# Performance work log

Measured on AMD Instinct MI355X. Metric: run time of the kernel, lower is better.

## Reference

```python
import jax, jax.numpy as jnp
import numpy as np
from math import ceil

WIDTH, HEIGHT, NUM_TILE = 1920, 1080, 16
# NOTE: original code computes BOTH block dims from height (bug preserved for faithfulness)
BLOCK_W = ceil(HEIGHT / NUM_TILE)
BLOCK_H = ceil(HEIGHT / NUM_TILE)
T = NUM_TILE * NUM_TILE  # 256 tiles
N = 65536


def setup_inputs() -> dict:
    key = jax.random.key(0)
    k1, k2, k3 = jax.random.split(key, 3)
    pos2d = jax.random.uniform(k1, (N, 2), jnp.float32) * jnp.array([WIDTH, HEIGHT], jnp.float32)
    radius = jax.random.uniform(k2, (N,), jnp.float32) * 2.0  # radius in tile units, avg ~3x3 tile footprint
    depth = jax.random.uniform(k3, (N,), jnp.float32) * 10.0
    return {"pos2d": pos2d, "radius": radius, "depth": depth}


def _tile_binning(pos2d, radius, depth):
    minval, maxval = 0.0, NUM_TILE - 1e-5
    xmin = jnp.clip(pos2d[:, 0] / BLOCK_W - radius, minval, maxval).astype(jnp.int32)
    xmax = jnp.clip(pos2d[:, 0] / BLOCK_W + radius, minval, maxval).astype(jnp.int32)
    ymin = jnp.clip(pos2d[:, 1] / BLOCK_H - radius, minval, maxval).astype(jnp.int32)
    ymax = jnp.clip(pos2d[:, 1] / BLOCK_H + radius, minval, maxval).astype(jnp.int32)

    tr = jnp.arange(NUM_TILE, dtype=jnp.int32)
    in_x = (tr[None, :] >= xmin[:, None]) & (tr[None, :] <= xmax[:, None])  # [N, 16]
    in_y = (tr[None, :] >= ymin[:, None]) & (tr[None, :] <= ymax[:, None])  # [N, 16]
    # tile index t = xi + NUM_TILE * yi  -> mask[n, yi, xi]
    mask = (in_y[:, :, None] & in_x[:, None, :]).reshape(N, T)  # [N, T]

    # inclusive-cumsum bucket offsets (matches torch.cumsum(tile_count))
    tile_count = jnp.cumsum(mask.sum(axis=0).astype(jnp.int32)).astype(jnp.int32)  # [T]
    total = tile_count[-1]

    # flattened entry list, tile-major then primitive-index order (matches scatter loop order)
    maskT = mask.T.reshape(-1)                                   # [T*N]
    tile_id = jnp.repeat(jnp.arange(T, dtype=jnp.int32), N)      # [T*N]
    prim_id = jnp.tile(jnp.arange(N, dtype=jnp.int32), T)        # [T*N]
    depth_e = depth[prim_id]
    tile_eff = jnp.where(maskT, tile_id, T)  # invalid entries pushed past all real tiles

    # segmented depth sort: primary key tile, secondary depth, tertiary prim (stable tiebreak)
    order = jnp.lexsort((prim_id, depth_e, tile_eff))
    prim_sorted = prim_id[order]
    valid = jnp.arange(T * N) < total
    tile_indices = jnp.where(valid, prim_sorted, -1).astype(jnp.int32)  # [T*N], -1 padded
    return tile_count, tile_indices


def reference(pos2d, radius, depth):
    # Equivalent of Screen.create_tiles(pos2d, radius) followed by Screen.depth_sort(depth).
    # Returns (tile_count: inclusive cumsum bucket offsets [T],
    #          tile_indices: per-tile depth-sorted primitive ids, padded to T*N with -1).
    return _tile_binning(pos2d, radius, depth)
```

## Files before the change

kernel.cpp:

```cpp
#include <hip/hip_runtime.h>
#include <hip/hip_bf16.h>
#include <stdint.h>

#define NPRIM 65536
#define NT 16
#define T_TILES 256
#define NBKT 2048
#define BCAP 256
#define CTHR 512
#define CBLK 512
#define FILLB (CBLK - T_TILES)

typedef unsigned long long u64;
typedef unsigned int u32;

__device__ __forceinline__ u32 dbucket(float d) {
    u32 b = (u32)(d * 204.8f);
    return b > (NBKT - 1) ? (NBKT - 1) : b;
}

__global__ __launch_bounds__(256) void k_compute(
    const float2* __restrict__ pos2d, const float* __restrict__ radius,
    const float* __restrict__ depth, u64* __restrict__ keysRaw,
    u32* __restrict__ bounds, u32* __restrict__ counts,
    u32* __restrict__ bucket_count)
{
    __shared__ u32 hist[T_TILES];
    __shared__ u32 bhist[NBKT];
    int tid = threadIdx.x;
    hist[tid] = 0;
    for (int j = tid; j < NBKT; j += 256) bhist[j] = 0;
    __syncthreads();

    int base = blockIdx.x * 1024;
    const float mx = (float)(16.0 - 1e-5);
    #pragma unroll
    for (int q = 0; q < 4; ++q) {
        int i = base + q * 256 + tid;
        float2 p = pos2d[i];
        float r = radius[i];
        float fx = p.x / 68.0f;
        float fy = p.y / 68.0f;
        int xmin = (int)fminf(fmaxf(fx - r, 0.0f), mx);
        int xmax = (int)fminf(fmaxf(fx + r, 0.0f), mx);
        int ymin = (int)fminf(fmaxf(fy - r, 0.0f), mx);
        int ymax = (int)fminf(fmaxf(fy + r, 0.0f), mx);
        bounds[i] = (u32)(xmin | (xmax << 4) | (ymin << 8) | (ymax << 12));
        float d = depth[i];
        keysRaw[i] = ((u64)__float_as_uint(d) << 16) | (u32)i;
        atomicAdd(&bhist[dbucket(d)], 1u);
        for (int ty = ymin; ty <= ymax; ++ty)
            for (int tx = xmin; tx <= xmax; ++tx)
                atomicAdd(&hist[ty * NT + tx], 1u);
    }
    __syncthreads();
    if (hist[tid]) atomicAdd(&counts[tid], hist[tid]);
    for (int j = tid; j < NBKT; j += 256)
        if (bhist[j]) atomicAdd(&bucket_count[j], bhist[j]);
}

__global__ __launch_bounds__(256) void k_scan(
    const u32* __restrict__ counts, const u32* __restrict__ bucket_count,
    int* __restrict__ tile_count, u32* __restrict__ offsets,
    u32* __restrict__ bucket_base, u32* __restrict__ cursor)
{
    __shared__ u32 wsum[4];
    int tid = threadIdx.x, lane = tid & 63, wave = tid >> 6;

    u32 c8[8]; u32 sum8 = 0;
    #pragma unroll
    for (int j = 0; j < 8; ++j) { c8[j] = bucket_count[tid * 8 + j]; sum8 += c8[j]; }
    u32 v = sum8;
    #pragma unroll
    for (int d = 1; d < 64; d <<= 1) {
        u32 t = __shfl_up(v, d, 64);
        if (lane >= d) v += t;
    }
    if (lane == 63) wsum[wave] = v;
    __syncthreads();
    u32 add = 0;
    for (int w = 0; w < wave; ++w) add += wsum[w];
    u32 run = v + add - sum8;
    #pragma unroll
    for (int j = 0; j < 8; ++j) {
        bucket_base[tid * 8 + j] = run;
        cursor[tid * 8 + j] = run;
        run += c8[j];
    }
    __syncthreads();

    u32 c = counts[tid];
    v = c;
    #pragma unroll
    for (int d = 1; d < 64; d <<= 1) {
        u32 t = __shfl_up(v, d, 64);
        if (lane >= d) v += t;
    }
    if (lane == 63) wsum[wave] = v;
    __syncthreads();
    add = 0;
    for (int w = 0; w < wave; ++w) add += wsum[w];
    v += add;
    tile_count[tid] = (int)v;
    offsets[tid] = v - c;
}

__global__ __launch_bounds__(256) void k_scatter(
    const u64* __restrict__ keysRaw, u32* __restrict__ cursor,
    u64* __restrict__ keysBkt)
{
    int base = blockIdx.x * 1024;
    int tid = threadIdx.x;
    #pragma unroll
    for (int q = 0; q < 4; ++q) {
        u64 key = keysRaw[base + q * 256 + tid];
        u32 d = dbucket(__uint_as_float((u32)(key >> 16)));
        u32 pos = atomicAdd(&cursor[d], 1u);
        keysBkt[pos] = key;
    }
}

__global__ __launch_bounds__(256) void k_bsort(
    const u64* __restrict__ keysBkt, const u32* __restrict__ bucket_base,
    const u32* __restrict__ bucket_count, const u32* __restrict__ bounds,
    u32* __restrict__ entries)
{
    __shared__ u64 buf[4][BCAP];
    int tid = threadIdx.x, lane = tid & 63, wave = tid >> 6;
    int bucket = blockIdx.x * 4 + wave;
    u32 base = bucket_base[bucket];
    u32 n = bucket_count[bucket];
    if (n > BCAP) n = BCAP;
    #pragma unroll
    for (int t = 0; t < 4; ++t) {
        u32 i = (u32)lane + 64u * t;
        if (i < n) buf[wave][i] = keysBkt[base + i];
    }
    __syncthreads();
    #pragma unroll
    for (int t = 0; t < 4; ++t) {
        u32 i = (u32)lane + 64u * t;
        if (i < n) {
            u64 ki = buf[wave][i];
            u32 r = 0;
            for (u32 j = 0; j < n; ++j) r += (buf[wave][j] < ki);
            u32 prim = (u32)ki & 0xFFFFu;
            entries[base + r] = (bounds[prim] << 16) | prim;
        }
    }
}

__global__ __launch_bounds__(CTHR) void k_compact(
    const uint4* __restrict__ entries4, const u32* __restrict__ offsets,
    const int* __restrict__ tile_count, int* __restrict__ out_idx)
{
    int b = blockIdx.x;
    int tid = threadIdx.x;

    if (b >= T_TILES) {
        u32 total = (u32)tile_count[T_TILES - 1];
        const u32 end = (u32)T_TILES * (u32)NPRIM;
        u32 s4 = (total + 3u) & ~3u;
        if (b == T_TILES && tid < (int)(s4 - total)) out_idx[total + tid] = -1;
        u32 n4 = (end - s4) >> 2;
        int4* o4 = (int4*)(out_idx + s4);
        int4 m1 = make_int4(-1, -1, -1, -1);
        u32 gid = (u32)(b - T_TILES) * (u32)CTHR + (u32)tid;
        for (u32 i = gid; i < n4; i += (u32)FILLB * (u32)CTHR) o4[i] = m1;
        return;
    }

    int tile = b;
    int tx = tile & 15, ty = tile >> 4;
    int lane = tid & 63, wave = tid >> 6;
    __shared__ u32 wtot[8];
    u32 base = offsets[tile];
    u64 lmask = (1ull << lane) - 1;

    for (int c = 0; c < NPRIM / 2048; ++c) {
        uint4 e = entries4[c * CTHR + tid];
        u32 ev[4] = {e.x, e.y, e.z, e.w};
        bool m[4]; u64 bal[4];
        #pragma unroll
        for (int q = 0; q < 4; ++q) {
            u32 bb = ev[q] >> 16;
            int xmn = bb & 15, xmx = (bb >> 4) & 15;
            int ymn = (bb >> 8) & 15, ymx = (bb >> 12) & 15;
            m[q] = (tx >= xmn) && (tx <= xmx) && (ty >= ymn) && (ty <= ymx);
            bal[q] = __ballot(m[q]);
        }
        u32 wcnt = __popcll(bal[0]) + __popcll(bal[1]) + __popcll(bal[2]) + __popcll(bal[3]);
        if (lane == 0) wtot[wave] = wcnt;
        __syncthreads();
        u32 woff = base, tot = 0;
        #pragma unroll
        for (int w = 0; w < 8; ++w) {
            u32 t = wtot[w];
            woff += (w < wave) ? t : 0;
            tot += t;
        }
        u32 pre = __popcll(bal[0] & lmask) + __popcll(bal[1] & lmask)
                + __popcll(bal[2] & lmask) + __popcll(bal[3] & lmask);
        #pragma unroll
        for (int q = 0; q < 4; ++q) {
            if (m[q]) { out_idx[woff + pre] = (int)(ev[q] & 0xFFFFu); pre++; }
        }
        base += tot;
        __syncthreads();
    }
}

extern "C" void kernel_launch(void* const* d_in, const int* in_sizes, int n_in,
                              void* d_out, int out_size, void* d_ws, size_t ws_size,
                              hipStream_t stream)
{
    const float2* pos2d  = (const float2*)d_in[0];
    const float*  radius = (const float*)d_in[1];
    const float*  depth  = (const float*)d_in[2];

    int* out32        = (int*)d_out;
    int* tile_count   = out32;
    int* tile_indices = out32 + T_TILES;

    char* ws = (char*)d_ws;
    u64* keysRaw = (u64*)(ws);
    u64* keysBkt = (u64*)(ws + 512 * 1024);
    u32* bounds  = (u32*)(ws + 1024 * 1024);
    u32* counts       = (u32*)(ws + 1280 * 1024);
    u32* bucket_count = (u32*)(ws + 1280 * 1024 + 4096);
    u32* offsets      = (u32*)(ws + 1280 * 1024 + 16384);
    u32* bucket_base  = (u32*)(ws + 1280 * 1024 + 20480);
    u32* cursor       = (u32*)(ws + 1280 * 1024 + 32768);

    (void)hipMemsetAsync(counts, 0, 12288, stream);

    k_compute<<<64, 256, 0, stream>>>(pos2d, radius, depth, keysRaw, bounds,
                                      counts, bucket_count);
    k_scan<<<1, 256, 0, stream>>>(counts, bucket_count, tile_count, offsets,
                                  bucket_base, cursor);
    k_scatter<<<64, 256, 0, stream>>>(keysRaw, cursor, keysBkt);

    u32* entries = (u32*)keysRaw;
    k_bsort<<<NBKT / 4, 256, 0, stream>>>(keysBkt, bucket_base, bucket_count,
                                          bounds, entries);
    k_compact<<<CBLK, CTHR, 0, stream>>>((const uint4*)entries, offsets,
                                         tile_count, tile_indices);
}
```

Before: 127.0 us.

## Replace global atomics and scan kernel with per-block histograms and deterministic scatter

k_compute now writes per-block tile and depth-bucket histograms instead of global atomics, and stores each key's local rank within its bucket in the key's upper bits. That removes the memset and the separate single-block scan kernel. k_scatter recomputes bucket offsets from the per-block histograms and places keys without global atomic cursors. k_compact reduces and scans the tile counts itself, and now does a two-pass count-then-write over wave-owned chunks, so the per-chunk block-wide barriers are gone. In exchange, every block redundantly reads all per-block histograms, and the entries are read twice in compaction.

```diff
diff --git a/kernel.cpp b/kernel.cpp
--- a/kernel.cpp
+++ b/kernel.cpp
@@ -1,5 +1,4 @@
 #include <hip/hip_runtime.h>
-#include <hip/hip_bf16.h>
 #include <stdint.h>
 
 #define NPRIM 65536
@@ -7,6 +6,7 @@
 #define T_TILES 256
 #define NBKT 2048
 #define BCAP 256
+#define NBLK 64
 #define CTHR 512
 #define CBLK 512
 #define FILLB (CBLK - T_TILES)
@@ -22,8 +22,8 @@
 __global__ __launch_bounds__(256) void k_compute(
     const float2* __restrict__ pos2d, const float* __restrict__ radius,
     const float* __restrict__ depth, u64* __restrict__ keysRaw,
-    u32* __restrict__ bounds, u32* __restrict__ counts,
-    u32* __restrict__ bucket_count)
+    u32* __restrict__ bounds, u32* __restrict__ counts_blk,
+    u32* __restrict__ bh)
 {
     __shared__ u32 hist[T_TILES];
     __shared__ u32 bhist[NBKT];
@@ -47,29 +47,42 @@
         int ymax = (int)fminf(fmaxf(fy + r, 0.0f), mx);
         bounds[i] = (u32)(xmin | (xmax << 4) | (ymin << 8) | (ymax << 12));
         float d = depth[i];
-        keysRaw[i] = ((u64)__float_as_uint(d) << 16) | (u32)i;
-        atomicAdd(&bhist[dbucket(d)], 1u);
+        u32 lrank = atomicAdd(&bhist[dbucket(d)], 1u);
+        keysRaw[i] = ((u64)lrank << 48) | ((u64)__float_as_uint(d) << 16) | (u32)i;
         for (int ty = ymin; ty <= ymax; ++ty)
             for (int tx = xmin; tx <= xmax; ++tx)
                 atomicAdd(&hist[ty * NT + tx], 1u);
     }
     __syncthreads();
-    if (hist[tid]) atomicAdd(&counts[tid], hist[tid]);
-    for (int j = tid; j < NBKT; j += 256)
-        if (bhist[j]) atomicAdd(&bucket_count[j], bhist[j]);
-}
-
-__global__ __launch_bounds__(256) void k_scan(
-    const u32* __restrict__ counts, const u32* __restrict__ bucket_count,
-    int* __restrict__ tile_count, u32* __restrict__ offsets,
-    u32* __restrict__ bucket_base, u32* __restrict__ cursor)
-{
+    counts_blk[blockIdx.x * 256 + tid] = hist[tid];
+    for (int j = tid; j < NBKT; j += 256) bh[blockIdx.x * NBKT + j] = bhist[j];
+}
+
+__global__ __launch_bounds__(256) void k_scatter(
+    const u64* __restrict__ keysRaw, const u32* __restrict__ bh,
+    u64* __restrict__ keysBkt, u32* __restrict__ bucket_base,
+    u32* __restrict__ bucket_count)
+{
+    __shared__ u32 loff[NBKT];
     __shared__ u32 wsum[4];
     int tid = threadIdx.x, lane = tid & 63, wave = tid >> 6;
-
-    u32 c8[8]; u32 sum8 = 0;
-    #pragma unroll
-    for (int j = 0; j < 8; ++j) { c8[j] = bucket_count[tid * 8 + j]; sum8 += c8[j]; }
+    int blk = blockIdx.x;
+
+    u32 c8[8] = {0,0,0,0,0,0,0,0};
+    u32 p8[8] = {0,0,0,0,0,0,0,0};
+    for (int b = 0; b < NBLK; ++b) {
+        const uint4* row = (const uint4*)(bh + b * NBKT + tid * 8);
+        uint4 h0 = row[0], h1 = row[1];
+        u32 h[8] = {h0.x, h0.y, h0.z, h0.w, h1.x, h1.y, h1.z, h1.w};
+        #pragma unroll
+        for (int j = 0; j < 8; ++j) {
+            if (b < blk) p8[j] += h[j];
+            c8[j] += h[j];
+        }
+    }
+    u32 sum8 = 0;
+    #pragma unroll
+    for (int j = 0; j < 8; ++j) sum8 += c8[j];
     u32 v = sum8;
     #pragma unroll
     for (int d = 1; d < 64; d <<= 1) {
@@ -83,40 +96,22 @@
     u32 run = v + add - sum8;
     #pragma unroll
     for (int j = 0; j < 8; ++j) {
-        bucket_base[tid * 8 + j] = run;
-        cursor[tid * 8 + j] = run;
+        loff[tid * 8 + j] = run + p8[j];
+        if (blk == 0) {
+            bucket_base[tid * 8 + j] = run;
+            bucket_count[tid * 8 + j] = c8[j];
+        }
         run += c8[j];
     }
     __syncthreads();
 
-    u32 c = counts[tid];
-    v = c;
-    #pragma unroll
-    for (int d = 1; d < 64; d <<= 1) {
-        u32 t = __shfl_up(v, d, 64);
-        if (lane >= d) v += t;
-    }
-    if (lane == 63) wsum[wave] = v;
-    __syncthreads();
-    add = 0;
-    for (int w = 0; w < wave; ++w) add += wsum[w];
-    v += add;
-    tile_count[tid] = (int)v;
-    offsets[tid] = v - c;
-}
-
-__global__ __launch_bounds__(256) void k_scatter(
-    const u64* __restrict__ keysRaw, u32* __restrict__ cursor,
-    u64* __restrict__ keysBkt)
-{
-    int base = blockIdx.x * 1024;
-    int tid = threadIdx.x;
+    int base = blk * 1024;
     #pragma unroll
     for (int q = 0; q < 4; ++q) {
         u64 key = keysRaw[base + q * 256 + tid];
         u32 d = dbucket(__uint_as_float((u32)(key >> 16)));
-        u32 pos = atomicAdd(&cursor[d], 1u);
-        keysBkt[pos] = key;
+        u32 lrank = (u32)(key >> 48);
+        keysBkt[loff[d] + lrank] = key & 0x0000FFFFFFFFFFFFull;
     }
 }
 
@@ -151,14 +146,45 @@
 }
 
 __global__ __launch_bounds__(CTHR) void k_compact(
-    const uint4* __restrict__ entries4, const u32* __restrict__ offsets,
-    const int* __restrict__ tile_count, int* __restrict__ out_idx)
-{
-    int b = blockIdx.x;
-    int tid = threadIdx.x;
+    const uint4* __restrict__ entries4, const u32* __restrict__ counts_blk,
+    int* __restrict__ tile_count, int* __restrict__ out_idx)
+{
+    __shared__ u32 cnt[T_TILES];
+    __shared__ u32 excl[T_TILES];
+    __shared__ u32 wsum[4];
+    __shared__ u32 chunkcnt[64];
+    __shared__ u32 chunkoff[64];
+    int b = blockIdx.x, tid = threadIdx.x, lane = tid & 63, wave = tid >> 6;
+
+    if (tid < 256) {
+        u32 s = 0;
+        for (int bb = 0; bb < NBLK; ++bb) s += counts_blk[bb * 256 + tid];
+        cnt[tid] = s;
+    }
+    __syncthreads();
+    if (tid < 256) {
+        u32 c = cnt[tid], v = c;
+        #pragma unroll
+        for (int d = 1; d < 64; d <<= 1) {
+            u32 t = __shfl_up(v, d, 64);
+            if (lane >= d) v += t;
+        }
+        if (lane == 63) wsum[wave] = v;
+        excl[tid] = v;
+    }
+    __syncthreads();
+    if (tid < 256) {
+        u32 add = 0;
+        for (int w = 0; w < wave; ++w) add += wsum[w];
+        u32 incl = excl[tid] + add;
+        excl[tid] = incl - cnt[tid];
+        cnt[tid] = incl;
+        if (b == 0) tile_count[tid] = (int)incl;
+    }
+    __syncthreads();
+    u32 total = cnt[T_TILES - 1];
 
     if (b >= T_TILES) {
-        u32 total = (u32)tile_count[T_TILES - 1];
         const u32 end = (u32)T_TILES * (u32)NPRIM;
         u32 s4 = (total + 3u) & ~3u;
         if (b == T_TILES && tid < (int)(s4 - total)) out_idx[total + tid] = -1;
@@ -170,43 +196,63 @@
         return;
     }
 
-    int tile = b;
-    int tx = tile & 15, ty = tile >> 4;
-    int lane = tid & 63, wave = tid >> 6;
-    __shared__ u32 wtot[8];
-    u32 base = offsets[tile];
+    int tile = b, tx = tile & 15, ty = tile >> 4;
+    u32 base0 = excl[tile];
     u64 lmask = (1ull << lane) - 1;
 
-    for (int c = 0; c < NPRIM / 2048; ++c) {
-        uint4 e = entries4[c * CTHR + tid];
-        u32 ev[4] = {e.x, e.y, e.z, e.w};
-        bool m[4]; u64 bal[4];
-        #pragma unroll
-        for (int q = 0; q < 4; ++q) {
-            u32 bb = ev[q] >> 16;
-            int xmn = bb & 15, xmx = (bb >> 4) & 15;
-            int ymn = (bb >> 8) & 15, ymx = (bb >> 12) & 15;
-            m[q] = (tx >= xmn) && (tx <= xmx) && (ty >= ymn) && (ty <= ymx);
-            bal[q] = __ballot(m[q]);
-        }
-        u32 wcnt = __popcll(bal[0]) + __popcll(bal[1]) + __popcll(bal[2]) + __popcll(bal[3]);
-        if (lane == 0) wtot[wave] = wcnt;
-        __syncthreads();
-        u32 woff = base, tot = 0;
-        #pragma unroll
-        for (int w = 0; w < 8; ++w) {
-            u32 t = wtot[w];
-            woff += (w < wave) ? t : 0;
-            tot += t;
-        }
-        u32 pre = __popcll(bal[0] & lmask) + __popcll(bal[1] & lmask)
-                + __popcll(bal[2] & lmask) + __popcll(bal[3] & lmask);
-        #pragma unroll
-        for (int q = 0; q < 4; ++q) {
-            if (m[q]) { out_idx[woff + pre] = (int)(ev[q] & 0xFFFFu); pre++; }
-        }
-        base += tot;
-        __syncthreads();
+    for (int cc = 0; cc < 8; ++cc) {
+        int ch = wave * 8 + cc;
+        u32 cs = 0;
+        #pragma unroll
+        for (int k = 0; k < 4; ++k) {
+            uint4 e = entries4[ch * 256 + k * 64 + lane];
+            u32 ev[4] = {e.x, e.y, e.z, e.w};
+            #pragma unroll
+            for (int q = 0; q < 4; ++q) {
+                u32 bb2 = ev[q] >> 16;
+                bool m = (tx >= (int)(bb2 & 15)) && (tx <= (int)((bb2 >> 4) & 15))
+                      && (ty >= (int)((bb2 >> 8) & 15)) && (ty <= (int)((bb2 >> 12) & 15));
+                cs += (u32)__popcll(__ballot(m));
+            }
+        }
+        if (lane == 0) chunkcnt[ch] = cs;
+    }
+    __syncthreads();
+    if (tid < 64) {
+        u32 c2 = chunkcnt[tid], v2 = c2;
+        #pragma unroll
+        for (int d = 1; d < 64; d <<= 1) {
+            u32 t = __shfl_up(v2, d, 64);
+            if (lane >= d) v2 += t;
+        }
+        chunkoff[tid] = base0 + v2 - c2;
+    }
+    __syncthreads();
+
+    for (int cc = 0; cc < 8; ++cc) {
+        int ch = wave * 8 + cc;
+        u32 run = chunkoff[ch];
+        #pragma unroll
+        for (int k = 0; k < 4; ++k) {
+            uint4 e = entries4[ch * 256 + k * 64 + lane];
+            u32 ev[4] = {e.x, e.y, e.z, e.w};
+            bool m[4]; u64 bal[4];
+            #pragma unroll
+            for (int q = 0; q < 4; ++q) {
+                u32 bb2 = ev[q] >> 16;
+                m[q] = (tx >= (int)(bb2 & 15)) && (tx <= (int)((bb2 >> 4) & 15))
+                    && (ty >= (int)((bb2 >> 8) & 15)) && (ty <= (int)((bb2 >> 12) & 15));
+                bal[q] = __ballot(m[q]);
+            }
+            u32 pre = (u32)(__popcll(bal[0] & lmask) + __popcll(bal[1] & lmask)
+                          + __popcll(bal[2] & lmask) + __popcll(bal[3] & lmask));
+            #pragma unroll
+            for (int q = 0; q < 4; ++q) {
+                if (m[q]) { out_idx[run + pre] = (int)(ev[q] & 0xFFFFu); pre++; }
+            }
+            run += (u32)(__popcll(bal[0]) + __popcll(bal[1])
+                       + __popcll(bal[2]) + __popcll(bal[3]));
+        }
     }
 }
 
@@ -223,26 +269,22 @@
     int* tile_indices = out32 + T_TILES;
 
     char* ws = (char*)d_ws;
-    u64* keysRaw = (u64*)(ws);
-    u64* keysBkt = (u64*)(ws + 512 * 1024);
-    u32* bounds  = (u32*)(ws + 1024 * 1024);
-    u32* counts       = (u32*)(ws + 1280 * 1024);
-    u32* bucket_count = (u32*)(ws + 1280 * 1024 + 4096);
-    u32* offsets      = (u32*)(ws + 1280 * 1024 + 16384);
-    u32* bucket_base  = (u32*)(ws + 1280 * 1024 + 20480);
-    u32* cursor       = (u32*)(ws + 1280 * 1024 + 32768);
-
-    (void)hipMemsetAsync(counts, 0, 12288, stream);
-
-    k_compute<<<64, 256, 0, stream>>>(pos2d, radius, depth, keysRaw, bounds,
-                                      counts, bucket_count);
-    k_scan<<<1, 256, 0, stream>>>(counts, bucket_count, tile_count, offsets,
-                                  bucket_base, cursor);
-    k_scatter<<<64, 256, 0, stream>>>(keysRaw, cursor, keysBkt);
+    u64* keysRaw      = (u64*)(ws);
+    u64* keysBkt      = (u64*)(ws + 512 * 1024);
+    u32* bounds       = (u32*)(ws + 1024 * 1024);
+    u32* counts_blk   = (u32*)(ws + 1280 * 1024);
+    u32* bh           = (u32*)(ws + 1344 * 1024);
+    u32* bucket_base  = (u32*)(ws + 1856 * 1024);
+    u32* bucket_count = (u32*)(ws + 1864 * 1024);
+
+    k_compute<<<NBLK, 256, 0, stream>>>(pos2d, radius, depth, keysRaw, bounds,
+                                        counts_blk, bh);
+    k_scatter<<<NBLK, 256, 0, stream>>>(keysRaw, bh, keysBkt,
+                                        bucket_base, bucket_count);
 
     u32* entries = (u32*)keysRaw;
     k_bsort<<<NBKT / 4, 256, 0, stream>>>(keysBkt, bucket_base, bucket_count,
                                           bounds, entries);
-    k_compact<<<CBLK, CTHR, 0, stream>>>((const uint4*)entries, offsets,
+    k_compact<<<CBLK, CTHR, 0, stream>>>((const uint4*)entries, counts_blk,
                                          tile_count, tile_indices);
 }
```

Result: slower. 145.5 us (+14.5%).
